# Optimization experiments

Measured on AMD Instinct MI355X. Metric: run time of the kernel, lower is better.

The kernel has to match this reference:

```python
import jax, jax.numpy as jnp
import numpy as np


def setup_inputs() -> dict:
    key = jax.random.key(0)
    k1, k2 = jax.random.split(key)
    B, S_ENC, S_DEC, D = 8, 4096, 4096, 256
    enc_output = jax.random.normal(k1, (B, S_ENC, D), dtype=jnp.float32)
    dec_output = jax.random.normal(k2, (B, S_DEC, D), dtype=jnp.float32)
    return {"enc_output": enc_output, "dec_output": dec_output}


def reference(enc_output, dec_output):
    # a_t[b, i, j] = <enc[b, i], dec[b, j]>  -> [B, S_enc, S_dec]
    a_t = jnp.einsum('bid,bjd->bij', enc_output, dec_output)
    # softmax over encoder positions (axis=1), matching torch.softmax(a_t, dim=1)
    a_t = jax.nn.softmax(a_t, axis=1)
    # c_t[b, j, d] = sum_i a_t[b, i, j] * enc[b, i, d]  -> [B, S_dec, D]
    c_t = jnp.einsum('bij,bid->bjd', a_t, enc_output)
    return c_t
```

## Files before the change

kernel.cpp:

```cpp
#include <hip/hip_runtime.h>

typedef unsigned short u16;
typedef unsigned int u32;
typedef __attribute__((ext_vector_type(8))) _Float16 half8;
typedef __attribute__((ext_vector_type(2))) __fp16 fp16x2;
typedef __attribute__((ext_vector_type(16))) float f32x16;

#define MFMA32(A, B, C) __builtin_amdgcn_mfma_f32_32x32x16_f16(A, B, C, 0, 0, 0)

constexpr int BN = 8;
constexpr int S = 4096;
constexpr int D = 256;
constexpr int KB = 32;
constexpr int NT = S / KB;
constexpr int TILE_U16 = KB * D;
constexpr int TP_U16 = 2 * TILE_U16;

__device__ __forceinline__ u32 pk2h(float a, float b) {
  union { _Float16 h[2]; u32 u; } x;
  x.h[0] = (_Float16)a; x.h[1] = (_Float16)b;
  return x.u;
}

__device__ __forceinline__ u32 pkrtz(float a, float b) {
  union { fp16x2 h; u32 u; } x;
  x.h = __builtin_amdgcn_cvt_pkrtz(a, b);
  return x.u;
}

__device__ __forceinline__ void gload_lds16(const void* g, void* l) {
  __builtin_amdgcn_global_load_lds((__attribute__((address_space(1))) void*)(void*)g,
                                   (__attribute__((address_space(3))) void*)l, 16, 0, 0);
}

__global__ __launch_bounds__(256) void convert_enc(const float* __restrict__ enc,
                                                   u16* __restrict__ ws) {
  const int blk = blockIdx.x;
  const int b = blk & 7;
  const int tp = blk >> 3;
  const int tid = threadIdx.x;

  const float* encb = enc + (size_t)b * S * D;

#pragma unroll
  for (int it = 0; it < 8; ++it) {
    int gg = it * 256 + tid;
    int t = tp * 2 + (gg >> 10);
    int g = gg & 1023;
    int i = g & 31;
    int ch = g >> 5;
    int d0 = ch * 8;
    const float* src = encb + (size_t)(t * 32 + i) * D + d0;
    float4 x = *(const float4*)src;
    float4 y = *(const float4*)(src + 4);
    uint4 o;
    o.x = pk2h(x.x, x.y); o.y = pk2h(x.z, x.w);
    o.z = pk2h(y.x, y.y); o.w = pk2h(y.z, y.w);
    *(uint4*)(ws + (size_t)(b * NT + t) * TP_U16 + g * 8) = o;
  }

  {
    int t = tp * 2 + (tid >> 7);
    int r = tid & 127;
    int o = r >> 5;
    int e = r & 31;
    int i0 = o * 8;
    int d0 = e * 8;
    float v[8][8];
#pragma unroll
    for (int rr = 0; rr < 8; ++rr) {
      const float* src = encb + (size_t)(t * 32 + i0 + rr) * D + d0;
      *(float4*)&v[rr][0] = *(const float4*)src;
      *(float4*)&v[rr][4] = *(const float4*)(src + 4);
    }
    int dsub = e >> 2;
    u16* dst = ws + (size_t)(b * NT + t) * TP_U16 + TILE_U16 +
               ((dsub * 4 + o) * 32 + (e & 3) * 8) * 8;
#pragma unroll
    for (int k = 0; k < 8; ++k) {
      uint4 q;
      q.x = pk2h(v[0][k], v[1][k]); q.y = pk2h(v[2][k], v[3][k]);
      q.z = pk2h(v[4][k], v[5][k]); q.w = pk2h(v[6][k], v[7][k]);
      *(uint4*)(dst + k * 8) = q;
    }
  }
}

__global__ __launch_bounds__(512, 2) void attn_kernel(const u16* __restrict__ ws_img,
                                                      const float* __restrict__ dec,
                                                      float* __restrict__ out) {
  __shared__ u16 LDSA[2][5][TILE_U16];

  const int tid = threadIdx.x;
  const int w = tid >> 6;
  const int wq = w & 3;
  const int kh = w >> 2;
  const int lane = tid & 63;
  const int h = lane >> 5;
  const int l31 = lane & 31;

  const int blk = blockIdx.x;
  const int b = blk & 7;
  const int q0 = (blk >> 3) << 7;
  const int qw = q0 + wq * 32;

  const u16* packs = ws_img + (size_t)b * NT * TP_U16;
  const float* decb = dec + (size_t)b * S * D;

  const float LOG2E = 1.4426950408889634f;
  half8 qf[16];
#pragma unroll
  for (int c = 0; c < 16; ++c) {
    const float* p = decb + (size_t)(qw + l31) * D + c * 16 + h * 8;
    float4 x = *(const float4*)p;
    float4 y = *(const float4*)(p + 4);
    union { u32 u[4]; half8 v; } uu;
    uu.u[0] = pk2h(x.x * LOG2E, x.y * LOG2E);
    uu.u[1] = pk2h(x.z * LOG2E, x.w * LOG2E);
    uu.u[2] = pk2h(y.x * LOG2E, y.y * LOG2E);
    uu.u[3] = pk2h(y.z * LOG2E, y.w * LOG2E);
    qf[c] = uu.v;
  }

  f32x16 acc[8] = {};
  float mrun = -1e30f;
  float lrun = 0.f;

  auto stagef = [&](int t, int eslot, int tslot) {
    const char* gs = (const char*)(packs + (size_t)t * TP_U16) +
                     (wq >> 1) * 16384 + (wq & 1) * 8192 + lane * 16;
    char* ls = (char*)&LDSA[kh][(wq < 2) ? eslot : (2 + tslot)][0] + (wq & 1) * 8192;
#pragma unroll
    for (int it = 0; it < 8; ++it)
      gload_lds16(gs + it * 1024, ls + it * 1024);
  };

  half8 bfrA[2];
  half8 bfrB[2];

  int e_cur = 0;
  int t_prev = 2, t_cur = 0, t_next = 1;

  stagef(kh, 0, 0);
  __syncthreads();

#pragma unroll 1
  for (int j = 0; j < 64; ++j) {
    if (j < 63) stagef(2 * (j + 1) + kh, e_cur ^ 1, t_next);

    f32x16 s0 = {}, s1 = {};
    {
      const char* eb = (const char*)&LDSA[kh][e_cur][0];
#pragma unroll
      for (int c = 0; c < 16; c += 2) {
        half8 a0 = *(const half8*)(eb + ((c + 0) * 2 + h) * 512 + l31 * 16);
        half8 a1 = *(const half8*)(eb + ((c + 1) * 2 + h) * 512 + l31 * 16);
        s0 = MFMA32(a0, qf[c + 0], s0);
        s1 = MFMA32(a1, qf[c + 1], s1);
      }
    }

    if (j > 0) {
      const char* tb = (const char*)&LDSA[kh][2 + t_prev][0];
#pragma unroll
      for (int ic = 0; ic < 2; ++ic) {
#pragma unroll
        for (int ds = 0; ds < 8; ++ds) {
          half8 vf = *(const half8*)(tb + ((ds * 2 + ic) * 2 + h) * 512 + l31 * 16);
          acc[ds] = MFMA32(vf, bfrA[ic], acc[ds]);
        }
      }
    }

    {
      f32x16 st = s0 + s1;
      float x0 = fmaxf(fmaxf(st[0], st[1]), fmaxf(st[2], st[3]));
      float x1 = fmaxf(fmaxf(st[4], st[5]), fmaxf(st[6], st[7]));
      float x2 = fmaxf(fmaxf(st[8], st[9]), fmaxf(st[10], st[11]));
      float x3 = fmaxf(fmaxf(st[12], st[13]), fmaxf(st[14], st[15]));
      float tm = fmaxf(fmaxf(x0, x1), fmaxf(x2, x3));
      tm = fmaxf(tm, __shfl_xor(tm, 32));
      if (__any(tm > mrun + 11.5f)) {
        float mnew = fmaxf(mrun, tm);
        float alpha = __builtin_amdgcn_exp2f(mrun - mnew);
        mrun = mnew;
        lrun *= alpha;
#pragma unroll
        for (int ds = 0; ds < 8; ++ds)
#pragma unroll
          for (int r = 0; r < 16; ++r) acc[ds][r] *= alpha;
      }
#pragma unroll
      for (int r = 0; r < 16; ++r) st[r] = __builtin_amdgcn_exp2f(st[r] - mrun);
      float y0 = (st[0] + st[1]) + (st[2] + st[3]);
      float y1 = (st[4] + st[5]) + (st[6] + st[7]);
      float y2 = (st[8] + st[9]) + (st[10] + st[11]);
      float y3 = (st[12] + st[13]) + (st[14] + st[15]);
      float rs = (y0 + y1) + (y2 + y3);
      rs += __shfl_xor(rs, 32);
      lrun += rs;

      u32 pkw[8];
#pragma unroll
      for (int rq = 0; rq < 4; ++rq) {
        pkw[rq * 2 + 0] = pkrtz(st[rq * 4 + 0], st[rq * 4 + 1]);
        pkw[rq * 2 + 1] = pkrtz(st[rq * 4 + 2], st[rq * 4 + 3]);
      }
#pragma unroll
      for (int ic = 0; ic < 2; ++ic) {
        u32 own0 = pkw[(2 * ic + h) * 2 + 0];
        u32 own1 = pkw[(2 * ic + h) * 2 + 1];
        u32 send0 = pkw[(2 * ic + 1 - h) * 2 + 0];
        u32 send1 = pkw[(2 * ic + 1 - h) * 2 + 1];
        u32 r0 = (u32)__shfl_xor((int)send0, 32);
        u32 r1 = (u32)__shfl_xor((int)send1, 32);
        union { u32 u[4]; half8 v; } bb;
        bb.u[0] = h ? r0 : own0;
        bb.u[1] = h ? r1 : own1;
        bb.u[2] = h ? own0 : r0;
        bb.u[3] = h ? own1 : r1;
        bfrB[ic] = bb.v;
      }
    }

    __syncthreads();

    bfrA[0] = bfrB[0]; bfrA[1] = bfrB[1];
    e_cur ^= 1;
    t_prev = t_cur; t_cur = t_next; t_next = (t_next == 2) ? 0 : t_next + 1;
  }

  {
    const char* tb = (const char*)&LDSA[kh][2 + t_prev][0];
#pragma unroll
    for (int ic = 0; ic < 2; ++ic) {
#pragma unroll
      for (int ds = 0; ds < 8; ++ds) {
        half8 vf = *(const half8*)(tb + ((ds * 2 + ic) * 2 + h) * 512 + l31 * 16);
        acc[ds] = MFMA32(vf, bfrA[ic], acc[ds]);
      }
    }
  }
  __syncthreads();

  float* fb = (float*)&LDSA[0][0][0];
  constexpr int XS = 20;
  float* mlb = fb + 30208;

  if (kh == 1) {
    if (lane < 32) {
      mlb[wq * 64 + lane] = mrun;
      mlb[wq * 64 + 32 + lane] = lrun;
    }
#pragma unroll
    for (int d4 = 0; d4 < 4; ++d4) {
      float* dst = fb + ((wq * 4 + d4) * 64 + lane) * XS;
#pragma unroll
      for (int r4 = 0; r4 < 4; ++r4) {
        float4 v;
        v.x = acc[d4][r4 * 4 + 0]; v.y = acc[d4][r4 * 4 + 1];
        v.z = acc[d4][r4 * 4 + 2]; v.w = acc[d4][r4 * 4 + 3];
        *(float4*)(dst + r4 * 4) = v;
      }
    }
  }
  __syncthreads();

  float a0 = 0.f, a1 = 0.f, inv = 0.f;
  const int q = qw + l31;
  float* orow = out + ((size_t)(b * S + q)) * D;
  if (kh == 0) {
    float m1 = mlb[wq * 64 + l31];
    float l1 = mlb[wq * 64 + 32 + l31];
    float mn = fmaxf(mrun, m1);
    a0 = __builtin_amdgcn_exp2f(mrun - mn);
    a1 = __builtin_amdgcn_exp2f(m1 - mn);
    inv = 1.0f / (a0 * lrun + a1 * l1);
#pragma unroll
    for (int d4 = 0; d4 < 4; ++d4) {
      const float* src = fb + ((wq * 4 + d4) * 64 + lane) * XS;
#pragma unroll
      for (int rq = 0; rq < 4; ++rq) {
        float4 u = *(const float4*)(src + rq * 4);
        int d = d4 * 32 + rq * 8 + h * 4;
        float4 o;
        o.x = (a0 * acc[d4][rq * 4 + 0] + a1 * u.x) * inv;
        o.y = (a0 * acc[d4][rq * 4 + 1] + a1 * u.y) * inv;
        o.z = (a0 * acc[d4][rq * 4 + 2] + a1 * u.z) * inv;
        o.w = (a0 * acc[d4][rq * 4 + 3] + a1 * u.w) * inv;
        *(float4*)(orow + d) = o;
      }
    }
  }
  __syncthreads();

  if (kh == 1) {
#pragma unroll
    for (int d4 = 0; d4 < 4; ++d4) {
      float* dst = fb + ((wq * 4 + d4) * 64 + lane) * XS;
#pragma unroll
      for (int r4 = 0; r4 < 4; ++r4) {
        float4 v;
        v.x = acc[d4 + 4][r4 * 4 + 0]; v.y = acc[d4 + 4][r4 * 4 + 1];
        v.z = acc[d4 + 4][r4 * 4 + 2]; v.w = acc[d4 + 4][r4 * 4 + 3];
        *(float4*)(dst + r4 * 4) = v;
      }
    }
  }
  __syncthreads();

  if (kh == 0) {
#pragma unroll
    for (int d4 = 0; d4 < 4; ++d4) {
      const float* src = fb + ((wq * 4 + d4) * 64 + lane) * XS;
#pragma unroll
      for (int rq = 0; rq < 4; ++rq) {
        float4 u = *(const float4*)(src + rq * 4);
        int d = (d4 + 4) * 32 + rq * 8 + h * 4;
        float4 o;
        o.x = (a0 * acc[d4 + 4][rq * 4 + 0] + a1 * u.x) * inv;
        o.y = (a0 * acc[d4 + 4][rq * 4 + 1] + a1 * u.y) * inv;
        o.z = (a0 * acc[d4 + 4][rq * 4 + 2] + a1 * u.z) * inv;
        o.w = (a0 * acc[d4 + 4][rq * 4 + 3] + a1 * u.w) * inv;
        *(float4*)(orow + d) = o;
      }
    }
  }
}

extern "C" void kernel_launch(void* const* d_in, const int* in_sizes, int n_in,
                              void* d_out, int out_size, void* d_ws, size_t ws_size,
                              hipStream_t stream) {
  const float* enc = (const float*)d_in[0];
  const float* dec = (const float*)d_in[1];
  float* out = (float*)d_out;

  u16* ws_img = (u16*)d_ws;

  convert_enc<<<BN * (S / 64), 256, 0, stream>>>(enc, ws_img);
  attn_kernel<<<BN * (S / 128), 512, 0, stream>>>(ws_img, dec, out);
}
```

Before: 192.5 us.

## Load MFMA operands directly from global memory instead of staging through LDS

```diff
diff --git a/kernel.cpp b/kernel.cpp
--- a/kernel.cpp
+++ b/kernel.cpp
@@ -26,11 +26,6 @@
   union { fp16x2 h; u32 u; } x;
   x.h = __builtin_amdgcn_cvt_pkrtz(a, b);
   return x.u;
-}
-
-__device__ __forceinline__ void gload_lds16(const void* g, void* l) {
-  __builtin_amdgcn_global_load_lds((__attribute__((address_space(1))) void*)(void*)g,
-                                   (__attribute__((address_space(3))) void*)l, 16, 0, 0);
 }
 
 __global__ __launch_bounds__(256) void convert_enc(const float* __restrict__ enc,
@@ -89,7 +84,7 @@
 __global__ __launch_bounds__(512, 2) void attn_kernel(const u16* __restrict__ ws_img,
                                                       const float* __restrict__ dec,
                                                       float* __restrict__ out) {
-  __shared__ u16 LDSA[2][5][TILE_U16];
+  __shared__ float fb[17680];
 
   const int tid = threadIdx.x;
   const int w = tid >> 6;
@@ -104,7 +99,7 @@
   const int q0 = (blk >> 3) << 7;
   const int qw = q0 + wq * 32;
 
-  const u16* packs = ws_img + (size_t)b * NT * TP_U16;
+  const char* packs = (const char*)(ws_img + (size_t)b * NT * TP_U16);
   const float* decb = dec + (size_t)b * S * D;
 
   const float LOG2E = 1.4426950408889634f;
@@ -126,126 +121,109 @@
   float mrun = -1e30f;
   float lrun = 0.f;
 
-  auto stagef = [&](int t, int eslot, int tslot) {
-    const char* gs = (const char*)(packs + (size_t)t * TP_U16) +
-                     (wq >> 1) * 16384 + (wq & 1) * 8192 + lane * 16;
-    char* ls = (char*)&LDSA[kh][(wq < 2) ? eslot : (2 + tslot)][0] + (wq & 1) * 8192;
-#pragma unroll
-    for (int it = 0; it < 8; ++it)
-      gload_lds16(gs + it * 1024, ls + it * 1024);
+  const int eoff = h * 512 + l31 * 16;
+
+  auto qkf = [&](int t) -> f32x16 {
+    const char* eb = packs + (size_t)t * 32768;
+    f32x16 s0 = {}, s1 = {};
+    __builtin_amdgcn_s_setprio(1);
+#pragma unroll
+    for (int c = 0; c < 16; c += 2) {
+      half8 a0 = *(const half8*)(eb + (c + 0) * 1024 + eoff);
+      half8 a1 = *(const half8*)(eb + (c + 1) * 1024 + eoff);
+      s0 = MFMA32(a0, qf[c + 0], s0);
+      s1 = MFMA32(a1, qf[c + 1], s1);
+    }
+    __builtin_amdgcn_s_setprio(0);
+    return s0 + s1;
   };
 
-  half8 bfrA[2];
-  half8 bfrB[2];
-
-  int e_cur = 0;
-  int t_prev = 2, t_cur = 0, t_next = 1;
-
-  stagef(kh, 0, 0);
+  auto pvf = [&](int t, const half8* bfr) {
+    const char* tb = packs + (size_t)t * 32768 + 16384;
+    __builtin_amdgcn_s_setprio(1);
+#pragma unroll
+    for (int ic = 0; ic < 2; ++ic) {
+#pragma unroll
+      for (int ds = 0; ds < 8; ++ds) {
+        half8 vf = *(const half8*)(tb + ((ds * 2 + ic) * 2) * 512 + eoff);
+        acc[ds] = MFMA32(vf, bfr[ic], acc[ds]);
+      }
+    }
+    __builtin_amdgcn_s_setprio(0);
+  };
+
+  auto smf = [&](f32x16 st, half8* bfr) {
+    float x0 = fmaxf(fmaxf(st[0], st[1]), fmaxf(st[2], st[3]));
+    float x1 = fmaxf(fmaxf(st[4], st[5]), fmaxf(st[6], st[7]));
+    float x2 = fmaxf(fmaxf(st[8], st[9]), fmaxf(st[10], st[11]));
+    float x3 = fmaxf(fmaxf(st[12], st[13]), fmaxf(st[14], st[15]));
+    float tm = fmaxf(fmaxf(x0, x1), fmaxf(x2, x3));
+    tm = fmaxf(tm, __shfl_xor(tm, 32));
+    if (__any(tm > mrun + 11.5f)) {
+      float mnew = fmaxf(mrun, tm);
+      float alpha = __builtin_amdgcn_exp2f(mrun - mnew);
+      mrun = mnew;
+      lrun *= alpha;
+#pragma unroll
+      for (int ds = 0; ds < 8; ++ds)
+#pragma unroll
+        for (int r = 0; r < 16; ++r) acc[ds][r] *= alpha;
+    }
+#pragma unroll
+    for (int r = 0; r < 16; ++r) st[r] = __builtin_amdgcn_exp2f(st[r] - mrun);
+    float y0 = (st[0] + st[1]) + (st[2] + st[3]);
+    float y1 = (st[4] + st[5]) + (st[6] + st[7]);
+    float y2 = (st[8] + st[9]) + (st[10] + st[11]);
+    float y3 = (st[12] + st[13]) + (st[14] + st[15]);
+    float rs = (y0 + y1) + (y2 + y3);
+    rs += __shfl_xor(rs, 32);
+    lrun += rs;
+
+    u32 pkw[8];
+#pragma unroll
+    for (int rq = 0; rq < 4; ++rq) {
+      pkw[rq * 2 + 0] = pkrtz(st[rq * 4 + 0], st[rq * 4 + 1]);
+      pkw[rq * 2 + 1] = pkrtz(st[rq * 4 + 2], st[rq * 4 + 3]);
+    }
+#pragma unroll
+    for (int ic = 0; ic < 2; ++ic) {
+      u32 own0 = pkw[(2 * ic + h) * 2 + 0];
+      u32 own1 = pkw[(2 * ic + h) * 2 + 1];
+      u32 send0 = pkw[(2 * ic + 1 - h) * 2 + 0];
+      u32 send1 = pkw[(2 * ic + 1 - h) * 2 + 1];
+      u32 r0 = (u32)__shfl_xor((int)send0, 32);
+      u32 r1 = (u32)__shfl_xor((int)send1, 32);
+      union { u32 u[4]; half8 v; } bb;
+      bb.u[0] = h ? r0 : own0;
+      bb.u[1] = h ? r1 : own1;
+      bb.u[2] = h ? own0 : r0;
+      bb.u[3] = h ? own1 : r1;
+      bfr[ic] = bb.v;
+    }
+  };
+
+  half8 bfrA[2], bfrB[2];
+
+  {
+    f32x16 st = qkf(kh);
+    smf(st, bfrA);
+  }
+
+#pragma unroll 1
+  for (int j = 1; j < 64; ++j) {
+    const int t = 2 * j + kh;
+    f32x16 st = qkf(t);
+    pvf(t - 2, bfrA);
+    smf(st, bfrB);
+    bfrA[0] = bfrB[0]; bfrA[1] = bfrB[1];
+  }
+
+  pvf(126 + kh, bfrA);
+
+  constexpr int XS = 17;
+  float* mlb = fb + 17408;
+
   __syncthreads();
-
-#pragma unroll 1
-  for (int j = 0; j < 64; ++j) {
-    if (j < 63) stagef(2 * (j + 1) + kh, e_cur ^ 1, t_next);
-
-    f32x16 s0 = {}, s1 = {};
-    {
-      const char* eb = (const char*)&LDSA[kh][e_cur][0];
-#pragma unroll
-      for (int c = 0; c < 16; c += 2) {
-        half8 a0 = *(const half8*)(eb + ((c + 0) * 2 + h) * 512 + l31 * 16);
-        half8 a1 = *(const half8*)(eb + ((c + 1) * 2 + h) * 512 + l31 * 16);
-        s0 = MFMA32(a0, qf[c + 0], s0);
-        s1 = MFMA32(a1, qf[c + 1], s1);
-      }
-    }
-
-    if (j > 0) {
-      const char* tb = (const char*)&LDSA[kh][2 + t_prev][0];
-#pragma unroll
-      for (int ic = 0; ic < 2; ++ic) {
-#pragma unroll
-        for (int ds = 0; ds < 8; ++ds) {
-          half8 vf = *(const half8*)(tb + ((ds * 2 + ic) * 2 + h) * 512 + l31 * 16);
-          acc[ds] = MFMA32(vf, bfrA[ic], acc[ds]);
-        }
-      }
-    }
-
-    {
-      f32x16 st = s0 + s1;
-      float x0 = fmaxf(fmaxf(st[0], st[1]), fmaxf(st[2], st[3]));
-      float x1 = fmaxf(fmaxf(st[4], st[5]), fmaxf(st[6], st[7]));
-      float x2 = fmaxf(fmaxf(st[8], st[9]), fmaxf(st[10], st[11]));
-      float x3 = fmaxf(fmaxf(st[12], st[13]), fmaxf(st[14], st[15]));
-      float tm = fmaxf(fmaxf(x0, x1), fmaxf(x2, x3));
-      tm = fmaxf(tm, __shfl_xor(tm, 32));
-      if (__any(tm > mrun + 11.5f)) {
-        float mnew = fmaxf(mrun, tm);
-        float alpha = __builtin_amdgcn_exp2f(mrun - mnew);
-        mrun = mnew;
-        lrun *= alpha;
-#pragma unroll
-        for (int ds = 0; ds < 8; ++ds)
-#pragma unroll
-          for (int r = 0; r < 16; ++r) acc[ds][r] *= alpha;
-      }
-#pragma unroll
-      for (int r = 0; r < 16; ++r) st[r] = __builtin_amdgcn_exp2f(st[r] - mrun);
-      float y0 = (st[0] + st[1]) + (st[2] + st[3]);
-      float y1 = (st[4] + st[5]) + (st[6] + st[7]);
-      float y2 = (st[8] + st[9]) + (st[10] + st[11]);
-      float y3 = (st[12] + st[13]) + (st[14] + st[15]);
-      float rs = (y0 + y1) + (y2 + y3);
-      rs += __shfl_xor(rs, 32);
-      lrun += rs;
-
-      u32 pkw[8];
-#pragma unroll
-      for (int rq = 0; rq < 4; ++rq) {
-        pkw[rq * 2 + 0] = pkrtz(st[rq * 4 + 0], st[rq * 4 + 1]);
-        pkw[rq * 2 + 1] = pkrtz(st[rq * 4 + 2], st[rq * 4 + 3]);
-      }
-#pragma unroll
-      for (int ic = 0; ic < 2; ++ic) {
-        u32 own0 = pkw[(2 * ic + h) * 2 + 0];
-        u32 own1 = pkw[(2 * ic + h) * 2 + 1];
-        u32 send0 = pkw[(2 * ic + 1 - h) * 2 + 0];
-        u32 send1 = pkw[(2 * ic + 1 - h) * 2 + 1];
-        u32 r0 = (u32)__shfl_xor((int)send0, 32);
-        u32 r1 = (u32)__shfl_xor((int)send1, 32);
-        union { u32 u[4]; half8 v; } bb;
-        bb.u[0] = h ? r0 : own0;
-        bb.u[1] = h ? r1 : own1;
-        bb.u[2] = h ? own0 : r0;
-        bb.u[3] = h ? own1 : r1;
-        bfrB[ic] = bb.v;
-      }
-    }
-
-    __syncthreads();
-
-    bfrA[0] = bfrB[0]; bfrA[1] = bfrB[1];
-    e_cur ^= 1;
-    t_prev = t_cur; t_cur = t_next; t_next = (t_next == 2) ? 0 : t_next + 1;
-  }
-
-  {
-    const char* tb = (const char*)&LDSA[kh][2 + t_prev][0];
-#pragma unroll
-    for (int ic = 0; ic < 2; ++ic) {
-#pragma unroll
-      for (int ds = 0; ds < 8; ++ds) {
-        half8 vf = *(const half8*)(tb + ((ds * 2 + ic) * 2 + h) * 512 + l31 * 16);
-        acc[ds] = MFMA32(vf, bfrA[ic], acc[ds]);
-      }
-    }
-  }
-  __syncthreads();
-
-  float* fb = (float*)&LDSA[0][0][0];
-  constexpr int XS = 20;
-  float* mlb = fb + 30208;
 
   if (kh == 1) {
     if (lane < 32) {
```

Result: slower. 581.3 us (+201.9%).

## Interleave QK and PV MFMAs in one loop with peeled first iteration

Applied to the files above, without the earlier changes.

```diff
diff --git a/kernel.cpp b/kernel.cpp
--- a/kernel.cpp
+++ b/kernel.cpp
@@ -126,6 +126,8 @@
   float mrun = -1e30f;
   float lrun = 0.f;
 
+  const int hoff = h * 512 + l31 * 16;
+
   auto stagef = [&](int t, int eslot, int tslot) {
     const char* gs = (const char*)(packs + (size_t)t * TP_U16) +
                      (wq >> 1) * 16384 + (wq & 1) * 8192 + lane * 16;
@@ -135,111 +137,124 @@
       gload_lds16(gs + it * 1024, ls + it * 1024);
   };
 
-  half8 bfrA[2];
-  half8 bfrB[2];
-
+  auto smf = [&](f32x16 st, half8* bfr) {
+    float x0 = fmaxf(fmaxf(st[0], st[1]), fmaxf(st[2], st[3]));
+    float x1 = fmaxf(fmaxf(st[4], st[5]), fmaxf(st[6], st[7]));
+    float x2 = fmaxf(fmaxf(st[8], st[9]), fmaxf(st[10], st[11]));
+    float x3 = fmaxf(fmaxf(st[12], st[13]), fmaxf(st[14], st[15]));
+    float tm = fmaxf(fmaxf(x0, x1), fmaxf(x2, x3));
+    tm = fmaxf(tm, __shfl_xor(tm, 32));
+    if (__any(tm > mrun + 11.5f)) {
+      float mnew = fmaxf(mrun, tm);
+      float alpha = __builtin_amdgcn_exp2f(mrun - mnew);
+      mrun = mnew;
+      lrun *= alpha;
+#pragma unroll
+      for (int ds = 0; ds < 8; ++ds)
+#pragma unroll
+        for (int r = 0; r < 16; ++r) acc[ds][r] *= alpha;
+    }
+#pragma unroll
+    for (int r = 0; r < 16; ++r) st[r] = __builtin_amdgcn_exp2f(st[r] - mrun);
+    float y0 = (st[0] + st[1]) + (st[2] + st[3]);
+    float y1 = (st[4] + st[5]) + (st[6] + st[7]);
+    float y2 = (st[8] + st[9]) + (st[10] + st[11]);
+    float y3 = (st[12] + st[13]) + (st[14] + st[15]);
+    float rs = (y0 + y1) + (y2 + y3);
+    rs += __shfl_xor(rs, 32);
+    lrun += rs;
+
+    u32 pkw[8];
+#pragma unroll
+    for (int rq = 0; rq < 4; ++rq) {
+      pkw[rq * 2 + 0] = pkrtz(st[rq * 4 + 0], st[rq * 4 + 1]);
+      pkw[rq * 2 + 1] = pkrtz(st[rq * 4 + 2], st[rq * 4 + 3]);
+    }
+#pragma unroll
+    for (int ic = 0; ic < 2; ++ic) {
+      u32 own0 = pkw[(2 * ic + h) * 2 + 0];
+      u32 own1 = pkw[(2 * ic + h) * 2 + 1];
+      u32 send0 = pkw[(2 * ic + 1 - h) * 2 + 0];
+      u32 send1 = pkw[(2 * ic + 1 - h) * 2 + 1];
+      u32 r0 = (u32)__shfl_xor((int)send0, 32);
+      u32 r1 = (u32)__shfl_xor((int)send1, 32);
+      union { u32 u[4]; half8 v; } bb;
+      bb.u[0] = h ? r0 : own0;
+      bb.u[1] = h ? r1 : own1;
+      bb.u[2] = h ? own0 : r0;
+      bb.u[3] = h ? own1 : r1;
+      bfr[ic] = bb.v;
+    }
+  };
+
+  half8 bfrA[2], bfrB[2];
   int e_cur = 0;
   int t_prev = 2, t_cur = 0, t_next = 1;
 
   stagef(kh, 0, 0);
   __syncthreads();
 
+  {
+    stagef(2 + kh, e_cur ^ 1, t_next);
+    const char* eb = (const char*)&LDSA[kh][e_cur][0];
+    f32x16 s0 = {}, s1 = {};
+    __builtin_amdgcn_s_setprio(1);
+#pragma unroll
+    for (int c = 0; c < 16; c += 2) {
+      half8 a0 = *(const half8*)(eb + (c + 0) * 1024 + hoff);
+      half8 a1 = *(const half8*)(eb + (c + 1) * 1024 + hoff);
+      s0 = MFMA32(a0, qf[c + 0], s0);
+      s1 = MFMA32(a1, qf[c + 1], s1);
+    }
+    __builtin_amdgcn_s_setprio(0);
+    smf(s0 + s1, bfrA);
+    __syncthreads();
+    e_cur ^= 1;
+    t_prev = t_cur; t_cur = t_next; t_next = (t_next == 2) ? 0 : t_next + 1;
+  }
+
 #pragma unroll 1
-  for (int j = 0; j < 64; ++j) {
+  for (int j = 1; j < 64; ++j) {
     if (j < 63) stagef(2 * (j + 1) + kh, e_cur ^ 1, t_next);
 
     f32x16 s0 = {}, s1 = {};
     {
       const char* eb = (const char*)&LDSA[kh][e_cur][0];
+      const char* tb = (const char*)&LDSA[kh][2 + t_prev][0];
+      __builtin_amdgcn_s_setprio(1);
 #pragma unroll
       for (int c = 0; c < 16; c += 2) {
-        half8 a0 = *(const half8*)(eb + ((c + 0) * 2 + h) * 512 + l31 * 16);
-        half8 a1 = *(const half8*)(eb + ((c + 1) * 2 + h) * 512 + l31 * 16);
+        half8 a0 = *(const half8*)(eb + (c + 0) * 1024 + hoff);
+        half8 a1 = *(const half8*)(eb + (c + 1) * 1024 + hoff);
+        half8 v0 = *(const half8*)(tb + (c + 0) * 1024 + hoff);
+        half8 v1 = *(const half8*)(tb + (c + 1) * 1024 + hoff);
         s0 = MFMA32(a0, qf[c + 0], s0);
         s1 = MFMA32(a1, qf[c + 1], s1);
-      }
-    }
-
-    if (j > 0) {
-      const char* tb = (const char*)&LDSA[kh][2 + t_prev][0];
-#pragma unroll
-      for (int ic = 0; ic < 2; ++ic) {
-#pragma unroll
-        for (int ds = 0; ds < 8; ++ds) {
-          half8 vf = *(const half8*)(tb + ((ds * 2 + ic) * 2 + h) * 512 + l31 * 16);
-          acc[ds] = MFMA32(vf, bfrA[ic], acc[ds]);
-        }
-      }
-    }
-
-    {
-      f32x16 st = s0 + s1;
-      float x0 = fmaxf(fmaxf(st[0], st[1]), fmaxf(st[2], st[3]));
-      float x1 = fmaxf(fmaxf(st[4], st[5]), fmaxf(st[6], st[7]));
-      float x2 = fmaxf(fmaxf(st[8], st[9]), fmaxf(st[10], st[11]));
-      float x3 = fmaxf(fmaxf(st[12], st[13]), fmaxf(st[14], st[15]));
-      float tm = fmaxf(fmaxf(x0, x1), fmaxf(x2, x3));
-      tm = fmaxf(tm, __shfl_xor(tm, 32));
-      if (__any(tm > mrun + 11.5f)) {
-        float mnew = fmaxf(mrun, tm);
-        float alpha = __builtin_amdgcn_exp2f(mrun - mnew);
-        mrun = mnew;
-        lrun *= alpha;
-#pragma unroll
-        for (int ds = 0; ds < 8; ++ds)
-#pragma unroll
-          for (int r = 0; r < 16; ++r) acc[ds][r] *= alpha;
-      }
-#pragma unroll
-      for (int r = 0; r < 16; ++r) st[r] = __builtin_amdgcn_exp2f(st[r] - mrun);
-      float y0 = (st[0] + st[1]) + (st[2] + st[3]);
-      float y1 = (st[4] + st[5]) + (st[6] + st[7]);
-      float y2 = (st[8] + st[9]) + (st[10] + st[11]);
-      float y3 = (st[12] + st[13]) + (st[14] + st[15]);
-      float rs = (y0 + y1) + (y2 + y3);
-      rs += __shfl_xor(rs, 32);
-      lrun += rs;
-
-      u32 pkw[8];
-#pragma unroll
-      for (int rq = 0; rq < 4; ++rq) {
-        pkw[rq * 2 + 0] = pkrtz(st[rq * 4 + 0], st[rq * 4 + 1]);
-        pkw[rq * 2 + 1] = pkrtz(st[rq * 4 + 2], st[rq * 4 + 3]);
-      }
-#pragma unroll
-      for (int ic = 0; ic < 2; ++ic) {
-        u32 own0 = pkw[(2 * ic + h) * 2 + 0];
-        u32 own1 = pkw[(2 * ic + h) * 2 + 1];
-        u32 send0 = pkw[(2 * ic + 1 - h) * 2 + 0];
-        u32 send1 = pkw[(2 * ic + 1 - h) * 2 + 1];
-        u32 r0 = (u32)__shfl_xor((int)send0, 32);
-        u32 r1 = (u32)__shfl_xor((int)send1, 32);
-        union { u32 u[4]; half8 v; } bb;
-        bb.u[0] = h ? r0 : own0;
-        bb.u[1] = h ? r1 : own1;
-        bb.u[2] = h ? own0 : r0;
-        bb.u[3] = h ? own1 : r1;
-        bfrB[ic] = bb.v;
-      }
-    }
+        acc[c >> 1] = MFMA32(v0, bfrA[0], acc[c >> 1]);
+        acc[c >> 1] = MFMA32(v1, bfrA[1], acc[c >> 1]);
+      }
+      __builtin_amdgcn_s_setprio(0);
+    }
+
+    smf(s0 + s1, bfrB);
+    bfrA[0] = bfrB[0]; bfrA[1] = bfrB[1];
 
     __syncthreads();
-
-    bfrA[0] = bfrB[0]; bfrA[1] = bfrB[1];
     e_cur ^= 1;
     t_prev = t_cur; t_cur = t_next; t_next = (t_next == 2) ? 0 : t_next + 1;
   }
 
   {
     const char* tb = (const char*)&LDSA[kh][2 + t_prev][0];
-#pragma unroll
-    for (int ic = 0; ic < 2; ++ic) {
-#pragma unroll
-      for (int ds = 0; ds < 8; ++ds) {
-        half8 vf = *(const half8*)(tb + ((ds * 2 + ic) * 2 + h) * 512 + l31 * 16);
-        acc[ds] = MFMA32(vf, bfrA[ic], acc[ds]);
-      }
-    }
+    __builtin_amdgcn_s_setprio(1);
+#pragma unroll
+    for (int c = 0; c < 16; c += 2) {
+      half8 v0 = *(const half8*)(tb + (c + 0) * 1024 + hoff);
+      half8 v1 = *(const half8*)(tb + (c + 1) * 1024 + hoff);
+      acc[c >> 1] = MFMA32(v0, bfrA[0], acc[c >> 1]);
+      acc[c >> 1] = MFMA32(v1, bfrA[1], acc[c >> 1]);
+    }
+    __builtin_amdgcn_s_setprio(0);
   }
   __syncthreads();
 
```

New measurement: 191.3 us. About the same (-0.7%).
